# Optimization experiments

Hardware: AMD Instinct MI355X
Metric: run time of the kernel (lower is better)

## Reference

```python
import jax, jax.numpy as jnp
import numpy as np

NUM_RAYS = 4096
NUM_SAMPLES = 64
NUM_IMPORTANCE = 64
UPSAMPLE_STEPS = 4
HIDDEN = 128
SAMPLE_DIST = 2.0 / NUM_SAMPLES
COS_ANNEAL_RATIO = 0.0


def sdf_fn(params, pts):
    # pts: [P,3] -> sdf: [P,1]  (stand-in for sdf_network.get_sdf_vals)
    W1, b1, W2, b2, W3, b3 = params
    h = jax.nn.softplus(pts @ W1 + b1)
    h = jax.nn.softplus(h @ W2 + b2)
    return h @ W3 + b3


def sdf_grad(params, pts):
    # gradient of sdf w.r.t. points, [P,3] (stand-in for sdf_network.gradient)
    return jax.grad(lambda p: sdf_fn(params, p).sum())(pts)


def sample_pdf(bins, weights, n_samples):
    # deterministic inverse-transform sampling (det=True branch)
    weights = weights + 1e-5
    pdf = weights / jnp.sum(weights, axis=-1, keepdims=True)
    cdf = jnp.cumsum(pdf, axis=-1)
    cdf = jnp.concatenate([jnp.zeros_like(cdf[..., :1]), cdf], axis=-1)  # [N,S]
    u = jnp.linspace(0.5 / n_samples, 1.0 - 0.5 / n_samples, n_samples, dtype=cdf.dtype)
    u = jnp.broadcast_to(u, cdf.shape[:-1] + (n_samples,))
    inds = jax.vmap(lambda c, uu: jnp.searchsorted(c, uu, side='right'))(cdf, u)
    below = jnp.maximum(inds - 1, 0)
    above = jnp.minimum(inds, cdf.shape[-1] - 1)
    cdf_b = jnp.take_along_axis(cdf, below, axis=-1)
    cdf_a = jnp.take_along_axis(cdf, above, axis=-1)
    bins_b = jnp.take_along_axis(bins, below, axis=-1)
    bins_a = jnp.take_along_axis(bins, above, axis=-1)
    denom = cdf_a - cdf_b
    denom = jnp.where(denom < 1e-5, jnp.ones_like(denom), denom)
    t = (u - cdf_b) / denom
    return bins_b + t * (bins_a - bins_b)


def upsample(rays_o, rays_d, z_vals, sdf, n_importance, inv_s):
    N, S = z_vals.shape
    pts = rays_o[:, None, :] + rays_d[:, None, :] * z_vals[..., None]  # [N,S,3]
    radius = jnp.linalg.norm(pts, axis=-1)
    inside_sphere = ((radius[:, :-1] < 1.0) | (radius[:, 1:] < 1.0)).astype(z_vals.dtype)
    prev_sdf, next_sdf = sdf[:, :-1], sdf[:, 1:]
    prev_z, next_z = z_vals[:, :-1], z_vals[:, 1:]
    mid_sdf = (prev_sdf + next_sdf) * 0.5
    cos_val = (next_sdf - prev_sdf) / (next_z - prev_z + 1e-5)
    prev_cos = jnp.concatenate([jnp.zeros((N, 1), z_vals.dtype), cos_val[:, :-1]], axis=-1)
    cos_val = jnp.minimum(prev_cos, cos_val)
    cos_val = jnp.clip(cos_val, -1000.0, 0.0) * inside_sphere
    dist = next_z - prev_z
    prev_cdf = jax.nn.sigmoid((mid_sdf - cos_val * dist * 0.5) * inv_s)
    next_cdf = jax.nn.sigmoid((mid_sdf + cos_val * dist * 0.5) * inv_s)
    alpha = (prev_cdf - next_cdf + 1e-5) / (prev_cdf + 1e-5)
    trans = jnp.cumprod(jnp.concatenate([jnp.ones((N, 1), z_vals.dtype), 1.0 - alpha + 1e-7], axis=-1), axis=-1)[:, :-1]
    weights = alpha * trans
    return sample_pdf(z_vals, weights, n_importance)


def cat_z_vals(params, rays_o, rays_d, z_vals, new_z_vals, sdf, last):
    N = z_vals.shape[0]
    z_cat = jnp.concatenate([z_vals, new_z_vals], axis=-1)
    order = jnp.argsort(z_cat, axis=-1)
    z_sorted = jnp.take_along_axis(z_cat, order, axis=-1)
    if not last:
        pts = rays_o[:, None, :] + rays_d[:, None, :] * new_z_vals[..., None]
        new_sdf = sdf_fn(params, pts.reshape(-1, 3)).reshape(N, new_z_vals.shape[-1])
        sdf = jnp.take_along_axis(jnp.concatenate([sdf, new_sdf], axis=-1), order, axis=-1)
    return z_sorted, sdf


def render_depth(params, variance, rays_o, rays_d, sample_dist, z_vals):
    N, S = z_vals.shape
    dists = z_vals[..., 1:] - z_vals[..., :-1]
    dists = jnp.concatenate([dists, jnp.full((N, 1), sample_dist, z_vals.dtype)], axis=-1)
    mid_z = z_vals + dists * 0.5
    pts = (rays_o[:, None, :] + rays_d[:, None, :] * mid_z[..., None]).reshape(-1, 3)
    dirs = jnp.broadcast_to(rays_d[:, None, :], (N, S, 3)).reshape(-1, 3)
    sdf = sdf_fn(params, pts)              # [P,1]
    gradients = sdf_grad(params, pts)      # [P,3]
    inv_s = jnp.clip(jnp.exp(10.0 * variance), 1e-6, 1e6)
    true_cos = jnp.sum(dirs * gradients, axis=-1, keepdims=True)
    iter_cos = -(jax.nn.relu(-true_cos * 0.5 + 0.5) * (1.0 - COS_ANNEAL_RATIO)
                 + jax.nn.relu(-true_cos) * COS_ANNEAL_RATIO)
    d = dists.reshape(-1, 1)
    prev_cdf = jax.nn.sigmoid((sdf - iter_cos * d * 0.5) * inv_s)
    next_cdf = jax.nn.sigmoid((sdf + iter_cos * d * 0.5) * inv_s)
    alpha = jnp.clip((prev_cdf - next_cdf + 1e-5) / (prev_cdf + 1e-5), 0.0, 1.0).reshape(N, S)
    trans = jnp.cumprod(jnp.concatenate([jnp.ones((N, 1), z_vals.dtype), 1.0 - alpha + 1e-7], axis=-1), axis=-1)[:, :-1]
    weights = alpha * trans
    depths = jnp.sum(weights * z_vals, axis=-1)
    return depths, gradients


def setup_inputs():
    key = jax.random.key(0)
    ks = jax.random.split(key, 8)
    rays_o = 0.1 * jax.random.normal(ks[0], (NUM_RAYS, 3), jnp.float32)
    rd = jax.random.normal(ks[1], (NUM_RAYS, 3), jnp.float32)
    rays_d = rd / jnp.linalg.norm(rd, axis=-1, keepdims=True)
    near = 0.3 + 0.2 * jax.random.uniform(ks[2], (NUM_RAYS, 1), jnp.float32)
    far = near + 1.5
    W1 = jax.random.normal(ks[3], (3, HIDDEN), jnp.float32) / np.sqrt(3.0)
    W2 = jax.random.normal(ks[4], (HIDDEN, HIDDEN), jnp.float32) / np.sqrt(HIDDEN)
    W3 = jax.random.normal(ks[5], (HIDDEN, 1), jnp.float32) / np.sqrt(HIDDEN)
    b1 = jnp.zeros((HIDDEN,), jnp.float32)
    b2 = jnp.zeros((HIDDEN,), jnp.float32)
    b3 = jnp.zeros((1,), jnp.float32)
    variance = jnp.asarray(0.3, jnp.float32)
    return {"rays_o": rays_o, "rays_d": rays_d, "near": near, "far": far,
            "W1": W1, "b1": b1, "W2": W2, "b2": b2, "W3": W3, "b3": b3,
            "variance": variance}


def reference(rays_o, rays_d, near, far, W1, b1, W2, b2, W3, b3, variance):
    params = (W1, b1, W2, b2, W3, b3)
    N = rays_o.shape[0]
    z = jnp.linspace(0.0, 1.0, NUM_SAMPLES, dtype=jnp.float32)
    z_vals = near + (far - near) * z[None, :]  # [N,S0]
    # importance sampling (torch.no_grad block)
    pts = rays_o[:, None, :] + rays_d[:, None, :] * z_vals[..., None]
    sdf = sdf_fn(params, pts.reshape(-1, 3)).reshape(N, NUM_SAMPLES)
    n_imp = NUM_IMPORTANCE // UPSAMPLE_STEPS
    for i in range(UPSAMPLE_STEPS):
        new_z = upsample(rays_o, rays_d, z_vals, sdf, n_imp, 64.0 * (2 ** i))
        z_vals, sdf = cat_z_vals(params, rays_o, rays_d, z_vals, new_z, sdf,
                                 last=(i + 1 == UPSAMPLE_STEPS))
    z_vals = jax.lax.stop_gradient(z_vals)
    return render_depth(params, variance, rays_o, rays_d, SAMPLE_DIST, z_vals)
```

## Files before the change

kernel.cpp:

```cpp
#include <hip/hip_runtime.h>
#include <math.h>

#define HID 128
#define NRAYS 4096
#define TP 64

typedef __bf16 bf16x8 __attribute__((ext_vector_type(8)));
typedef float f32x4 __attribute__((ext_vector_type(4)));
typedef unsigned int uint32x4 __attribute__((ext_vector_type(4)));

union frag_u { bf16x8 v; uint32x4 q; };

__device__ __forceinline__ unsigned f2bf(float f){
  unsigned u = __float_as_uint(f);
  u += 0x7FFFu + ((u >> 16) & 1u);
  return u >> 16;
}
__device__ __forceinline__ float bf2f(unsigned h){
  return __uint_as_float(h << 16);
}
__device__ __forceinline__ float sp_fast(float x){
  float e = __expf(-fabsf(x));
  return fmaxf(x, 0.0f) + __logf(1.0f + e);
}
__device__ __forceinline__ float sg_fast(float x){
  float e = __expf(-fabsf(x));
  float r = __builtin_amdgcn_rcpf(1.0f + e);
  return (x >= 0.0f ? 1.0f : e) * r;
}
__device__ __forceinline__ float sg_f(float x){
  return 1.0f / (1.0f + expf(-x));
}
__device__ __forceinline__ f32x4 splat4(float x){
  f32x4 v = {x, x, x, x};
  return v;
}

#define SW(p,k) ((((p)*HID) + (k)) ^ (((p)&7)<<3))

__global__ void k_make_frags(const float* __restrict__ W2,
    unsigned short* __restrict__ w2fh,  unsigned short* __restrict__ w2fl,
    unsigned short* __restrict__ w2tfh, unsigned short* __restrict__ w2tfl){
  int idx = blockIdx.x*256 + threadIdx.x;
  if (idx >= 4096) return;
  int which = idx >> 11;
  int f    = (idx >> 6) & 31;
  int lane = idx & 63;
  int kc = f >> 3, tg = f & 7;
  int lg = lane >> 4, lr = lane & 15;
  unsigned short* dh = which ? w2tfh : w2fh;
  unsigned short* dl = which ? w2tfl : w2fl;
  int base = (f*64 + lane)*8;
  #pragma unroll
  for (int e = 0; e < 8; e++){
    int a = 32*kc + 8*lg + e;
    int b = 16*tg + lr;
    float v = which ? W2[b*HID + a] : W2[a*HID + b];
    unsigned hi = f2bf(v);
    dh[base+e] = (unsigned short)hi;
    dl[base+e] = (unsigned short)f2bf(v - bf2f(hi));
  }
}

__global__ void k_make_frags3(const float* __restrict__ W2,
    unsigned short* __restrict__ dh, unsigned short* __restrict__ dm,
    unsigned short* __restrict__ dl){
  int idx = blockIdx.x*256 + threadIdx.x;
  if (idx >= 2048) return;
  int f    = idx >> 6;
  int lane = idx & 63;
  int kc = f >> 3, tg = f & 7;
  int lg = lane >> 4, lr = lane & 15;
  int base = (f*64 + lane)*8;
  #pragma unroll
  for (int e = 0; e < 8; e++){
    int a = 32*kc + 8*lg + e;
    int b = 16*tg + lr;
    float v = W2[a*HID + b];
    unsigned hi = f2bf(v);
    float rm = v - bf2f(hi);
    unsigned md = f2bf(rm);
    dh[base+e] = (unsigned short)hi;
    dm[base+e] = (unsigned short)md;
    dl[base+e] = (unsigned short)f2bf(rm - bf2f(md));
  }
}

__global__ void k_init(const float* __restrict__ rays_o, const float* __restrict__ rays_d,
                       const float* __restrict__ nearv, const float* __restrict__ farv,
                       float* __restrict__ z_buf, float* __restrict__ pts){
  int idx = blockIdx.x*256 + threadIdx.x;
  if (idx >= NRAYS*64) return;
  int ray = idx >> 6, j = idx & 63;
  float nr = nearv[ray];
  float z = nr + (farv[ray] - nr) * ((float)j / 63.0f);
  z_buf[ray*128 + j] = z;
  pts[idx*3+0] = rays_o[ray*3+0] + rays_d[ray*3+0]*z;
  pts[idx*3+1] = rays_o[ray*3+1] + rays_d[ray*3+1]*z;
  pts[idx*3+2] = rays_o[ray*3+2] + rays_d[ray*3+2]*z;
}

__global__ __launch_bounds__(256, 3) void k_mlp_fwd_t(
    const float* __restrict__ pts,
    const float* __restrict__ W1, const float* __restrict__ b1,
    const float* __restrict__ b2,
    const float* __restrict__ W3, const float* __restrict__ b3,
    const unsigned short* __restrict__ w2h, const unsigned short* __restrict__ w2m,
    const unsigned short* __restrict__ w2l,
    float* __restrict__ sdf_out, const int* __restrict__ slots, int mode)
{
  __shared__ unsigned short sHi[64*HID];
  __shared__ unsigned short sMi[64*HID];
  __shared__ unsigned short sLo[64*HID];
  __shared__ float sRed[4][64];

  const int tid = threadIdx.x;
  const int l   = tid & 63;
  const int wv  = __builtin_amdgcn_readfirstlane(tid >> 6);
  const int lg  = l >> 4;
  const int lr  = l & 15;
  const int q0  = blockIdx.x * 64;
  const int kb  = 32*wv;

  const float x0 = pts[(q0+l)*3+0];
  const float x1 = pts[(q0+l)*3+1];
  const float x2 = pts[(q0+l)*3+2];

  #pragma unroll
  for (int g = 0; g < 4; g++){
    unsigned hw[4], mw[4], lw[4];
    #pragma unroll
    for (int e2 = 0; e2 < 4; e2++){
      unsigned hpk[2], mpk[2], lpk[2];
      #pragma unroll
      for (int t = 0; t < 2; t++){
        int k = kb + 8*g + 2*e2 + t;
        float pre = b1[k];
        pre = fmaf(x0, W1[k],       pre);
        pre = fmaf(x1, W1[HID+k],   pre);
        pre = fmaf(x2, W1[2*HID+k], pre);
        float h = sp_fast(pre);
        unsigned hi = f2bf(h);
        float rm = h - bf2f(hi);
        unsigned md = f2bf(rm);
        hpk[t] = hi; mpk[t] = md;
        lpk[t] = f2bf(rm - bf2f(md));
      }
      hw[e2] = hpk[0] | (hpk[1] << 16);
      mw[e2] = mpk[0] | (mpk[1] << 16);
      lw[e2] = lpk[0] | (lpk[1] << 16);
    }
    uint32x4 hq = {hw[0], hw[1], hw[2], hw[3]};
    uint32x4 mq = {mw[0], mw[1], mw[2], mw[3]};
    uint32x4 lq = {lw[0], lw[1], lw[2], lw[3]};
    *(uint32x4*)&sHi[SW(l, kb + 8*g)] = hq;
    *(uint32x4*)&sMi[SW(l, kb + 8*g)] = mq;
    *(uint32x4*)&sLo[SW(l, kb + 8*g)] = lq;
  }
  __syncthreads();

  f32x4 acc[4][2], accC[4][2];
  {
    const float b2a = b2[kb + lr];
    const float b2b = b2[kb + 16 + lr];
    #pragma unroll
    for (int mt = 0; mt < 4; mt++){
      acc[mt][0]  = splat4(b2a);
      acc[mt][1]  = splat4(b2b);
      accC[mt][0] = splat4(0.0f);
      accC[mt][1] = splat4(0.0f);
    }
  }
  #pragma unroll
  for (int kc = 0; kc < 4; kc++){
    frag_u bh0, bm0, bl0, bh1, bm1, bl1;
    const int f0 = ((kc*8 + 2*wv + 0)*64 + l)*8;
    const int f1 = ((kc*8 + 2*wv + 1)*64 + l)*8;
    bh0.q = *(const uint32x4*)(w2h + f0);
    bm0.q = *(const uint32x4*)(w2m + f0);
    bl0.q = *(const uint32x4*)(w2l + f0);
    bh1.q = *(const uint32x4*)(w2h + f1);
    bm1.q = *(const uint32x4*)(w2m + f1);
    bl1.q = *(const uint32x4*)(w2l + f1);
    const int kk = 32*kc + 8*lg;
    #pragma unroll
    for (int mt = 0; mt < 4; mt++){
      frag_u ah, am, al;
      ah.q = *(const uint32x4*)&sHi[SW(16*mt + lr, kk)];
      am.q = *(const uint32x4*)&sMi[SW(16*mt + lr, kk)];
      al.q = *(const uint32x4*)&sLo[SW(16*mt + lr, kk)];
      accC[mt][0] = __builtin_amdgcn_mfma_f32_16x16x32_bf16(ah.v, bl0.v, accC[mt][0], 0,0,0);
      accC[mt][0] = __builtin_amdgcn_mfma_f32_16x16x32_bf16(am.v, bm0.v, accC[mt][0], 0,0,0);
      accC[mt][0] = __builtin_amdgcn_mfma_f32_16x16x32_bf16(al.v, bh0.v, accC[mt][0], 0,0,0);
      accC[mt][0] = __builtin_amdgcn_mfma_f32_16x16x32_bf16(ah.v, bm0.v, accC[mt][0], 0,0,0);
      accC[mt][0] = __builtin_amdgcn_mfma_f32_16x16x32_bf16(am.v, bh0.v, accC[mt][0], 0,0,0);
      acc[mt][0]  = __builtin_amdgcn_mfma_f32_16x16x32_bf16(ah.v, bh0.v, acc[mt][0],  0,0,0);
      accC[mt][1] = __builtin_amdgcn_mfma_f32_16x16x32_bf16(ah.v, bl1.v, accC[mt][1], 0,0,0);
      accC[mt][1] = __builtin_amdgcn_mfma_f32_16x16x32_bf16(am.v, bm1.v, accC[mt][1], 0,0,0);
      accC[mt][1] = __builtin_amdgcn_mfma_f32_16x16x32_bf16(al.v, bh1.v, accC[mt][1], 0,0,0);
      accC[mt][1] = __builtin_amdgcn_mfma_f32_16x16x32_bf16(ah.v, bm1.v, accC[mt][1], 0,0,0);
      accC[mt][1] = __builtin_amdgcn_mfma_f32_16x16x32_bf16(am.v, bh1.v, accC[mt][1], 0,0,0);
      acc[mt][1]  = __builtin_amdgcn_mfma_f32_16x16x32_bf16(ah.v, bh1.v, acc[mt][1],  0,0,0);
    }
  }

  {
    const float w3a = W3[kb + lr];
    const float w3b = W3[kb + 16 + lr];
    #pragma unroll
    for (int mt = 0; mt < 4; mt++){
      float svr[4];
      #pragma unroll
      for (int r = 0; r < 4; r++){
        float pa = acc[mt][0][r] + accC[mt][0][r];
        float pb = acc[mt][1][r] + accC[mt][1][r];
        svr[r] = sp_fast(pa)*w3a + sp_fast(pb)*w3b;
      }
      #pragma unroll
      for (int m = 1; m < 16; m <<= 1){
        svr[0] += __shfl_xor(svr[0], m);
        svr[1] += __shfl_xor(svr[1], m);
        svr[2] += __shfl_xor(svr[2], m);
        svr[3] += __shfl_xor(svr[3], m);
      }
      if (lr == 0){
        sRed[wv][16*mt + 4*lg + 0] = svr[0];
        sRed[wv][16*mt + 4*lg + 1] = svr[1];
        sRed[wv][16*mt + 4*lg + 2] = svr[2];
        sRed[wv][16*mt + 4*lg + 3] = svr[3];
      }
    }
  }
  __syncthreads();
  if (tid < 64){
    float sv = b3[0] + sRed[0][tid] + sRed[1][tid] + sRed[2][tid] + sRed[3][tid];
    if (mode == 0){
      sdf_out[q0 + tid] = sv;
    } else if (mode == 1){
      sdf_out[(q0 << 1) + tid] = sv;
    } else {
      int p = q0 + tid;
      sdf_out[(p >> 4)*128 + slots[p]] = sv;
    }
  }
}

__global__ __launch_bounds__(256, 4) void k_mlp_bwd(
    const float* __restrict__ z_buf,
    const float* __restrict__ rays_o, const float* __restrict__ rays_d,
    const float* __restrict__ W1, const float* __restrict__ b1,
    const float* __restrict__ b2,
    const float* __restrict__ W3, const float* __restrict__ b3,
    const unsigned short* __restrict__ w2fh,  const unsigned short* __restrict__ w2fl,
    const unsigned short* __restrict__ w2tfh,
    float* __restrict__ sdf_out, float* __restrict__ grad_out)
{
  __shared__ unsigned short sHi[64*HID];
  __shared__ unsigned short sLo[64*HID];
  __shared__ float sRed[4][64];
  __shared__ float sPts[64][4];
  __shared__ float sGrad[4][64][3];

  const int tid = threadIdx.x;
  const int l   = tid & 63;
  const int wv  = __builtin_amdgcn_readfirstlane(tid >> 6);
  const int lg  = l >> 4;
  const int lr  = l & 15;
  const int q0  = blockIdx.x * 64;
  const int kb  = 32*wv;

  const int ray = q0 >> 7;
  const int s   = (q0 & 127) + l;
  const float z  = z_buf[q0 + l];
  const float zn = z_buf[q0 + l + ((s < 127) ? 1 : 0)];
  const float d  = (s < 127) ? (zn - z) : 0.03125f;
  const float midz = z + 0.5f*d;
  const float x0 = rays_o[ray*3+0] + rays_d[ray*3+0]*midz;
  const float x1 = rays_o[ray*3+1] + rays_d[ray*3+1]*midz;
  const float x2 = rays_o[ray*3+2] + rays_d[ray*3+2]*midz;
  if (wv == 0){ sPts[l][0] = x0; sPts[l][1] = x1; sPts[l][2] = x2; }

  #pragma unroll
  for (int g = 0; g < 4; g++){
    unsigned hw[4], lw[4];
    #pragma unroll
    for (int e2 = 0; e2 < 4; e2++){
      unsigned hpk[2], lpk[2];
      #pragma unroll
      for (int t = 0; t < 2; t++){
        int k = kb + 8*g + 2*e2 + t;
        float pre = b1[k];
        pre = fmaf(x0, W1[k],       pre);
        pre = fmaf(x1, W1[HID+k],   pre);
        pre = fmaf(x2, W1[2*HID+k], pre);
        float h = sp_fast(pre);
        unsigned hi = __float_as_uint(h) >> 16;
        float rm = h - __uint_as_float(hi << 16);
        hpk[t] = hi;
        lpk[t] = __float_as_uint(rm) >> 16;
      }
      hw[e2] = hpk[0] | (hpk[1] << 16);
      lw[e2] = lpk[0] | (lpk[1] << 16);
    }
    uint32x4 hq = {hw[0], hw[1], hw[2], hw[3]};
    uint32x4 lq = {lw[0], lw[1], lw[2], lw[3]};
    *(uint32x4*)&sHi[SW(l, kb + 8*g)] = hq;
    *(uint32x4*)&sLo[SW(l, kb + 8*g)] = lq;
  }
  __syncthreads();

  f32x4 acc[4][2];
  {
    const float b2a = b2[kb + lr];
    const float b2b = b2[kb + 16 + lr];
    #pragma unroll
    for (int mt = 0; mt < 4; mt++){
      acc[mt][0] = splat4(b2a);
      acc[mt][1] = splat4(b2b);
    }
  }
  #pragma unroll
  for (int kc = 0; kc < 4; kc++){
    frag_u bh0, bl0, bh1, bl1;
    const int f0 = ((kc*8 + 2*wv + 0)*64 + l)*8;
    const int f1 = ((kc*8 + 2*wv + 1)*64 + l)*8;
    bh0.q = *(const uint32x4*)(w2fh + f0);
    bl0.q = *(const uint32x4*)(w2fl + f0);
    bh1.q = *(const uint32x4*)(w2fh + f1);
    bl1.q = *(const uint32x4*)(w2fl + f1);
    const int kk = 32*kc + 8*lg;
    #pragma unroll
    for (int mt = 0; mt < 4; mt++){
      frag_u ah, al;
      ah.q = *(const uint32x4*)&sHi[SW(16*mt + lr, kk)];
      al.q = *(const uint32x4*)&sLo[SW(16*mt + lr, kk)];
      acc[mt][0] = __builtin_amdgcn_mfma_f32_16x16x32_bf16(ah.v, bh0.v, acc[mt][0], 0,0,0);
      acc[mt][0] = __builtin_amdgcn_mfma_f32_16x16x32_bf16(ah.v, bl0.v, acc[mt][0], 0,0,0);
      acc[mt][0] = __builtin_amdgcn_mfma_f32_16x16x32_bf16(al.v, bh0.v, acc[mt][0], 0,0,0);
      acc[mt][1] = __builtin_amdgcn_mfma_f32_16x16x32_bf16(ah.v, bh1.v, acc[mt][1], 0,0,0);
      acc[mt][1] = __builtin_amdgcn_mfma_f32_16x16x32_bf16(ah.v, bl1.v, acc[mt][1], 0,0,0);
      acc[mt][1] = __builtin_amdgcn_mfma_f32_16x16x32_bf16(al.v, bh1.v, acc[mt][1], 0,0,0);
    }
  }
  __syncthreads();

  {
    const float w3a = W3[kb + lr];
    const float w3b = W3[kb + 16 + lr];
    #pragma unroll
    for (int mt = 0; mt < 4; mt++){
      float svr[4];
      #pragma unroll
      for (int r = 0; r < 4; r++){
        float pa = acc[mt][0][r], pb = acc[mt][1][r];
        svr[r] = sp_fast(pa)*w3a + sp_fast(pb)*w3b;
        int pr = 16*mt + 4*lg + r;
        float ga = sg_fast(pa) * w3a;
        float gb = sg_fast(pb) * w3b;
        sHi[SW(pr, kb + lr)]      = (unsigned short)(__float_as_uint(ga) >> 16);
        sHi[SW(pr, kb + 16 + lr)] = (unsigned short)(__float_as_uint(gb) >> 16);
      }
      #pragma unroll
      for (int m = 1; m < 16; m <<= 1){
        svr[0] += __shfl_xor(svr[0], m);
        svr[1] += __shfl_xor(svr[1], m);
        svr[2] += __shfl_xor(svr[2], m);
        svr[3] += __shfl_xor(svr[3], m);
      }
      if (lr == 0){
        sRed[wv][16*mt + 4*lg + 0] = svr[0];
        sRed[wv][16*mt + 4*lg + 1] = svr[1];
        sRed[wv][16*mt + 4*lg + 2] = svr[2];
        sRed[wv][16*mt + 4*lg + 3] = svr[3];
      }
    }
  }
  __syncthreads();
  if (tid < 64)
    sdf_out[q0+tid] = b3[0] + sRed[0][tid] + sRed[1][tid] + sRed[2][tid] + sRed[3][tid];

  f32x4 acc2[4][2];
  #pragma unroll
  for (int pt = 0; pt < 4; pt++){
    acc2[pt][0] = splat4(0.0f);
    acc2[pt][1] = splat4(0.0f);
  }
  #pragma unroll
  for (int kcn = 0; kcn < 4; kcn++){
    frag_u ah0, ah1;
    const int f0 = ((kcn*8 + 2*wv + 0)*64 + l)*8;
    const int f1 = ((kcn*8 + 2*wv + 1)*64 + l)*8;
    ah0.q = *(const uint32x4*)(w2tfh + f0);
    ah1.q = *(const uint32x4*)(w2tfh + f1);
    const int nn = 32*kcn + 8*lg;
    #pragma unroll
    for (int pt = 0; pt < 4; pt++){
      frag_u bh;
      bh.q = *(const uint32x4*)&sHi[SW(16*pt + lr, nn)];
      acc2[pt][0] = __builtin_amdgcn_mfma_f32_16x16x32_bf16(ah0.v, bh.v, acc2[pt][0], 0,0,0);
      acc2[pt][1] = __builtin_amdgcn_mfma_f32_16x16x32_bf16(ah1.v, bh.v, acc2[pt][1], 0,0,0);
    }
  }

  {
    float w1a[2][4], w1b[2][4], w1c[2][4], b1v[2][4];
    #pragma unroll
    for (int t = 0; t < 2; t++)
      #pragma unroll
      for (int r = 0; r < 4; r++){
        int k = kb + 16*t + 4*lg + r;
        w1a[t][r] = W1[k]; w1b[t][r] = W1[HID+k]; w1c[t][r] = W1[2*HID+k];
        b1v[t][r] = b1[k];
      }
    #pragma unroll
    for (int pt = 0; pt < 4; pt++){
      const int p = 16*pt + lr;
      const float xx = sPts[p][0], xy = sPts[p][1], xz = sPts[p][2];
      float gx = 0.f, gy = 0.f, gz = 0.f;
      #pragma unroll
      for (int t = 0; t < 2; t++){
        #pragma unroll
        for (int r = 0; r < 4; r++){
          float pre1 = fmaf(xx, w1a[t][r], fmaf(xy, w1b[t][r], fmaf(xz, w1c[t][r], b1v[t][r])));
          float dp = acc2[pt][t][r] * sg_fast(pre1);
          gx = fmaf(w1a[t][r], dp, gx);
          gy = fmaf(w1b[t][r], dp, gy);
          gz = fmaf(w1c[t][r], dp, gz);
        }
      }
      gx += __shfl_xor(gx, 16); gx += __shfl_xor(gx, 32);
      gy += __shfl_xor(gy, 16); gy += __shfl_xor(gy, 32);
      gz += __shfl_xor(gz, 16); gz += __shfl_xor(gz, 32);
      if (lg == 0){
        sGrad[wv][p][0] = gx; sGrad[wv][p][1] = gy; sGrad[wv][p][2] = gz;
      }
    }
  }
  __syncthreads();
  if (tid < 64){
    #pragma unroll
    for (int c = 0; c < 3; c++)
      grad_out[(q0+tid)*3+c] =
        sGrad[0][tid][c] + sGrad[1][tid][c] + sGrad[2][tid][c] + sGrad[3][tid][c];
  }
}

__global__ __launch_bounds__(64) void k_upsample(
      const float* __restrict__ rays_o, const float* __restrict__ rays_d,
      float* __restrict__ z_buf, float* __restrict__ sdf_buf,
      float* __restrict__ pts_new, int* __restrict__ slots,
      int S, float inv_s, int last){
  __shared__ float z[128], sd[128], rad[128], cosv[128], alf[128], wv[128], cdf[129], nz[16];
  __shared__ int slt[16];
  const int ray = blockIdx.x;
  const int l   = threadIdx.x;
  const float ox = rays_o[ray*3], oy = rays_o[ray*3+1], oz = rays_o[ray*3+2];
  const float dx = rays_d[ray*3], dy = rays_d[ray*3+1], dz = rays_d[ray*3+2];
  for (int j = l; j < S; j += 64){
    float zz = z_buf[ray*128+j];
    z[j]  = zz;
    sd[j] = sdf_buf[ray*128+j];
    float px = ox+dx*zz, py = oy+dy*zz, pz = oz+dz*zz;
    rad[j] = sqrtf(px*px + py*py + pz*pz);
  }
  __syncthreads();
  for (int j = l; j < S-1; j += 64)
    cosv[j] = (sd[j+1]-sd[j]) / (z[j+1]-z[j] + 1e-5f);
  __syncthreads();
  for (int j = l; j < S-1; j += 64){
    float cv = fminf((j > 0) ? cosv[j-1] : 0.0f, cosv[j]);
    cv = fminf(fmaxf(cv, -1000.0f), 0.0f);
    float inside = (rad[j] < 1.0f || rad[j+1] < 1.0f) ? 1.0f : 0.0f;
    cv *= inside;
    float mid  = 0.5f*(sd[j]+sd[j+1]);
    float dist = z[j+1]-z[j];
    float e = sg_f((mid - cv*dist*0.5f)*inv_s);
    float f = sg_f((mid + cv*dist*0.5f)*inv_s);
    alf[j] = (e - f + 1e-5f) / (e + 1e-5f);
  }
  __syncthreads();
  if (l == 0){
    float T = 1.0f, wsum = 0.0f;
    for (int j = 0; j < S-1; j++){
      float w = alf[j]*T + 1e-5f;
      wv[j] = w; wsum += w;
      T *= (1.0f - alf[j] + 1e-7f);
    }
    cdf[0] = 0.0f;
    float c = 0.0f;
    for (int j = 0; j < S-1; j++){ c += wv[j]/wsum; cdf[j+1] = c; }
  }
  __syncthreads();
  if (l < 16){
    float u = 0.03125f + 0.0625f*(float)l;
    int idx = 0;
    while (idx < S && cdf[idx] <= u) idx++;
    int below = idx - 1; if (below < 0) below = 0;
    int above = (idx < S-1) ? idx : (S-1);
    float cb = cdf[below], ca = cdf[above];
    float den = ca - cb; if (den < 1e-5f) den = 1.0f;
    float t = (u - cb) / den;
    nz[l] = z[below] + t*(z[above] - z[below]);
  }
  __syncthreads();
  if (l == 0){
    int i = S-1, j = 15;
    for (int dst = S+15; dst >= 0; --dst){
      bool takeOld = (j < 0) || (i >= 0 && z[i] > nz[j]);
      if (takeOld){ z[dst] = z[i]; sd[dst] = sd[i]; i--; }
      else        { z[dst] = nz[j]; slt[j] = dst; j--; }
    }
  }
  __syncthreads();
  for (int j = l; j < S+16; j += 64){
    z_buf[ray*128+j]  = z[j];
    sdf_buf[ray*128+j] = sd[j];
  }
  if (!last && l < 16){
    slots[ray*16+l] = slt[l];
    float zz = nz[l];
    pts_new[(ray*16+l)*3+0] = ox + dx*zz;
    pts_new[(ray*16+l)*3+1] = oy + dy*zz;
    pts_new[(ray*16+l)*3+2] = oz + dz*zz;
  }
}

__global__ __launch_bounds__(64) void k_render(
    const float* __restrict__ z_buf, const float* __restrict__ sdf_mid,
    const float* __restrict__ rays_d, const float* __restrict__ grad,
    const float* __restrict__ variance, float* __restrict__ depth_out){
  const int ray = blockIdx.x;
  const int l   = threadIdx.x;
  float inv_s = expf(10.0f * variance[0]);
  inv_s = fminf(fmaxf(inv_s, 1e-6f), 1e6f);
  const float dx = rays_d[ray*3], dy = rays_d[ray*3+1], dz = rays_d[ray*3+2];
  const int i0 = ray*128 + 2*l, i1 = i0 + 1;
  const float z0 = z_buf[i0], z1 = z_buf[i1];
  const float zn1 = __shfl_down(z0, 1);
  const float d0 = z1 - z0;
  const float d1 = (l < 63) ? (zn1 - z1) : 0.03125f;
  float a0, a1;
  {
    float sdf = sdf_mid[i0];
    float gx = grad[i0*3], gy = grad[i0*3+1], gz = grad[i0*3+2];
    float tc = dx*gx + dy*gy + dz*gz;
    float ic = -fmaxf(0.5f - 0.5f*tc, 0.0f);
    float e = sg_fast((sdf - ic*d0*0.5f)*inv_s);
    float f = sg_fast((sdf + ic*d0*0.5f)*inv_s);
    a0 = fminf(fmaxf((e - f + 1e-5f) / (e + 1e-5f), 0.0f), 1.0f);
  }
  {
    float sdf = sdf_mid[i1];
    float gx = grad[i1*3], gy = grad[i1*3+1], gz = grad[i1*3+2];
    float tc = dx*gx + dy*gy + dz*gz;
    float ic = -fmaxf(0.5f - 0.5f*tc, 0.0f);
    float e = sg_fast((sdf - ic*d1*0.5f)*inv_s);
    float f = sg_fast((sdf + ic*d1*0.5f)*inv_s);
    a1 = fminf(fmaxf((e - f + 1e-5f) / (e + 1e-5f), 0.0f), 1.0f);
  }
  const float f0 = 1.0f - a0 + 1e-7f;
  const float f1 = 1.0f - a1 + 1e-7f;
  float incl = f0 * f1;
  #pragma unroll
  for (int off = 1; off < 64; off <<= 1){
    float t = __shfl_up(incl, off);
    if (l >= off) incl *= t;
  }
  float P = __shfl_up(incl, 1);
  if (l == 0) P = 1.0f;
  float part = P * (a0*z0 + f0*a1*z1);
  #pragma unroll
  for (int m = 1; m < 64; m <<= 1) part += __shfl_xor(part, m);
  if (l == 0) depth_out[ray] = part;
}

extern "C" void kernel_launch(void* const* d_in, const int* in_sizes, int n_in,
                              void* d_out, int out_size, void* d_ws, size_t ws_size,
                              hipStream_t stream){
  (void)in_sizes; (void)n_in; (void)out_size; (void)ws_size;
  const float* rays_o = (const float*)d_in[0];
  const float* rays_d = (const float*)d_in[1];
  const float* nearv  = (const float*)d_in[2];
  const float* farv   = (const float*)d_in[3];
  const float* W1 = (const float*)d_in[4];
  const float* b1 = (const float*)d_in[5];
  const float* W2 = (const float*)d_in[6];
  const float* b2 = (const float*)d_in[7];
  const float* W3 = (const float*)d_in[8];
  const float* b3 = (const float*)d_in[9];
  const float* variance = (const float*)d_in[10];

  float* ws      = (float*)d_ws;
  float* z_buf   = ws;
  float* sdf_buf = ws + 524288;
  float* sdf_tmp = ws + 1048576;
  int*   slots   = (int*)(ws + 1589248);
  unsigned short* w2fh  = (unsigned short*)(ws + 524288);
  unsigned short* w2fl  = w2fh + 16384;
  unsigned short* w2tfh = w2fh + 32768;
  unsigned short* w2tfl = w2fh + 49152;
  unsigned short* w2h3 = (unsigned short*)(ws + 1310720);
  unsigned short* w2m3 = w2h3 + 16384;
  unsigned short* w2l3 = w2h3 + 32768;

  float* out       = (float*)d_out;
  float* depth_out = out;
  float* grad_out  = out + NRAYS;
  float* pts       = grad_out;

  k_make_frags3<<<dim3(8), dim3(256), 0, stream>>>(W2, w2h3, w2m3, w2l3);
  k_init<<<dim3(1024), dim3(256), 0, stream>>>(rays_o, rays_d, nearv, farv, z_buf, pts);
  k_mlp_fwd_t<<<dim3(4096), dim3(256), 0, stream>>>(pts, W1,b1,b2,W3,b3,
                                                    w2h3,w2m3,w2l3, sdf_buf, nullptr, 1);

  for (int i = 0; i < 4; i++){
    int S = 64 + 16*i;
    float inv_s = (float)(64 << i);
    int last = (i == 3) ? 1 : 0;
    k_upsample<<<dim3(4096), dim3(64), 0, stream>>>(rays_o, rays_d, z_buf, sdf_buf,
                                                    pts, slots, S, inv_s, last);
    if (!last){
      k_mlp_fwd_t<<<dim3(1024), dim3(256), 0, stream>>>(pts, W1,b1,b2,W3,b3,
                                                        w2h3,w2m3,w2l3, sdf_buf, slots, 2);
    }
  }

  k_make_frags<<<dim3(16), dim3(256), 0, stream>>>(W2, w2fh, w2fl, w2tfh, w2tfl);
  k_mlp_bwd<<<dim3(8192), dim3(256), 0, stream>>>(z_buf, rays_o, rays_d,
                                                  W1,b1,b2,W3,b3,
                                                  w2fh,w2fl,w2tfh, sdf_tmp, grad_out);
  k_render<<<dim3(4096), dim3(64), 0, stream>>>(z_buf, sdf_tmp, rays_d, grad_out,
                                                variance, depth_out);
}
```

Measured before the change: 544.7 us.

## Fuse ray init into first MLP pass and use hardware bf16 conversions

Removes the separate k_init kernel. The first forward MLP pass (mode 1) now computes the initial z values and sample points directly from near/far and the ray data, and writes z_buf itself. Manual round-to-nearest bf16 packing and truncation are replaced with native __bf16 casts, which may map to hardware conversion instructions. The softplus and sigmoid evaluations in the backward kernel now share one exp per value. The truncations that became rounded conversions slightly change numerics in the split-precision backward path.

Result: no change. 540.8 us (-0.7%).

```diff
diff --git a/kernel.cpp b/kernel.cpp
--- a/kernel.cpp
+++ b/kernel.cpp
@@ -18,6 +18,11 @@
 }
 __device__ __forceinline__ float bf2f(unsigned h){
   return __uint_as_float(h << 16);
+}
+__device__ __forceinline__ unsigned short bfc(float f){
+  union { __bf16 b; unsigned short u; } c;
+  c.b = (__bf16)f;
+  return c.u;
 }
 __device__ __forceinline__ float sp_fast(float x){
   float e = __expf(-fabsf(x));
@@ -86,22 +91,11 @@
   }
 }
 
-__global__ void k_init(const float* __restrict__ rays_o, const float* __restrict__ rays_d,
-                       const float* __restrict__ nearv, const float* __restrict__ farv,
-                       float* __restrict__ z_buf, float* __restrict__ pts){
-  int idx = blockIdx.x*256 + threadIdx.x;
-  if (idx >= NRAYS*64) return;
-  int ray = idx >> 6, j = idx & 63;
-  float nr = nearv[ray];
-  float z = nr + (farv[ray] - nr) * ((float)j / 63.0f);
-  z_buf[ray*128 + j] = z;
-  pts[idx*3+0] = rays_o[ray*3+0] + rays_d[ray*3+0]*z;
-  pts[idx*3+1] = rays_o[ray*3+1] + rays_d[ray*3+1]*z;
-  pts[idx*3+2] = rays_o[ray*3+2] + rays_d[ray*3+2]*z;
-}
-
 __global__ __launch_bounds__(256, 3) void k_mlp_fwd_t(
     const float* __restrict__ pts,
+    const float* __restrict__ rays_o, const float* __restrict__ rays_d,
+    const float* __restrict__ nearv, const float* __restrict__ farv,
+    float* __restrict__ z_buf,
     const float* __restrict__ W1, const float* __restrict__ b1,
     const float* __restrict__ b2,
     const float* __restrict__ W3, const float* __restrict__ b3,
@@ -122,16 +116,27 @@
   const int q0  = blockIdx.x * 64;
   const int kb  = 32*wv;
 
-  const float x0 = pts[(q0+l)*3+0];
-  const float x1 = pts[(q0+l)*3+1];
-  const float x2 = pts[(q0+l)*3+2];
+  float x0, x1, x2;
+  if (mode == 1){
+    const int ray = blockIdx.x;
+    float nr = nearv[ray];
+    float z  = nr + (farv[ray] - nr) * ((float)l / 63.0f);
+    x0 = rays_o[ray*3+0] + rays_d[ray*3+0]*z;
+    x1 = rays_o[ray*3+1] + rays_d[ray*3+1]*z;
+    x2 = rays_o[ray*3+2] + rays_d[ray*3+2]*z;
+    if (wv == 0) z_buf[ray*128 + l] = z;
+  } else {
+    x0 = pts[(q0+l)*3+0];
+    x1 = pts[(q0+l)*3+1];
+    x2 = pts[(q0+l)*3+2];
+  }
 
   #pragma unroll
   for (int g = 0; g < 4; g++){
     unsigned hw[4], mw[4], lw[4];
     #pragma unroll
     for (int e2 = 0; e2 < 4; e2++){
-      unsigned hpk[2], mpk[2], lpk[2];
+      unsigned short hpk[2], mpk[2], lpk[2];
       #pragma unroll
       for (int t = 0; t < 2; t++){
         int k = kb + 8*g + 2*e2 + t;
@@ -140,15 +145,15 @@
         pre = fmaf(x1, W1[HID+k],   pre);
         pre = fmaf(x2, W1[2*HID+k], pre);
         float h = sp_fast(pre);
-        unsigned hi = f2bf(h);
-        float rm = h - bf2f(hi);
-        unsigned md = f2bf(rm);
-        hpk[t] = hi; mpk[t] = md;
-        lpk[t] = f2bf(rm - bf2f(md));
-      }
-      hw[e2] = hpk[0] | (hpk[1] << 16);
-      mw[e2] = mpk[0] | (mpk[1] << 16);
-      lw[e2] = lpk[0] | (lpk[1] << 16);
+        unsigned short hh = bfc(h);
+        float rm = h - bf2f(hh);
+        unsigned short mm = bfc(rm);
+        hpk[t] = hh; mpk[t] = mm;
+        lpk[t] = bfc(rm - bf2f(mm));
+      }
+      hw[e2] = (unsigned)hpk[0] | ((unsigned)hpk[1] << 16);
+      mw[e2] = (unsigned)mpk[0] | ((unsigned)mpk[1] << 16);
+      lw[e2] = (unsigned)lpk[0] | ((unsigned)lpk[1] << 16);
     }
     uint32x4 hq = {hw[0], hw[1], hw[2], hw[3]};
     uint32x4 mq = {mw[0], mw[1], mw[2], mw[3]};
@@ -285,7 +290,7 @@
     unsigned hw[4], lw[4];
     #pragma unroll
     for (int e2 = 0; e2 < 4; e2++){
-      unsigned hpk[2], lpk[2];
+      unsigned short hpk[2], lpk[2];
       #pragma unroll
       for (int t = 0; t < 2; t++){
         int k = kb + 8*g + 2*e2 + t;
@@ -294,13 +299,12 @@
         pre = fmaf(x1, W1[HID+k],   pre);
         pre = fmaf(x2, W1[2*HID+k], pre);
         float h = sp_fast(pre);
-        unsigned hi = __float_as_uint(h) >> 16;
-        float rm = h - __uint_as_float(hi << 16);
-        hpk[t] = hi;
-        lpk[t] = __float_as_uint(rm) >> 16;
-      }
-      hw[e2] = hpk[0] | (hpk[1] << 16);
-      lw[e2] = lpk[0] | (lpk[1] << 16);
+        unsigned short hh = bfc(h);
+        hpk[t] = hh;
+        lpk[t] = bfc(h - bf2f(hh));
+      }
+      hw[e2] = (unsigned)hpk[0] | ((unsigned)hpk[1] << 16);
+      lw[e2] = (unsigned)lpk[0] | ((unsigned)lpk[1] << 16);
     }
     uint32x4 hq = {hw[0], hw[1], hw[2], hw[3]};
     uint32x4 lq = {lw[0], lw[1], lw[2], lw[3]};
@@ -353,12 +357,16 @@
       #pragma unroll
       for (int r = 0; r < 4; r++){
         float pa = acc[mt][0][r], pb = acc[mt][1][r];
-        svr[r] = sp_fast(pa)*w3a + sp_fast(pb)*w3b;
+        float ea = __expf(-fabsf(pa)), eb = __expf(-fabsf(pb));
+        float ta = 1.0f + ea,          tb = 1.0f + eb;
+        float spa = fmaxf(pa, 0.0f) + __logf(ta);
+        float spb = fmaxf(pb, 0.0f) + __logf(tb);
+        svr[r] = spa*w3a + spb*w3b;
+        float sga = (pa >= 0.0f ? 1.0f : ea) * __builtin_amdgcn_rcpf(ta);
+        float sgb = (pb >= 0.0f ? 1.0f : eb) * __builtin_amdgcn_rcpf(tb);
         int pr = 16*mt + 4*lg + r;
-        float ga = sg_fast(pa) * w3a;
-        float gb = sg_fast(pb) * w3b;
-        sHi[SW(pr, kb + lr)]      = (unsigned short)(__float_as_uint(ga) >> 16);
-        sHi[SW(pr, kb + 16 + lr)] = (unsigned short)(__float_as_uint(gb) >> 16);
+        sHi[SW(pr, kb + lr)]      = bfc(sga * w3a);
+        sHi[SW(pr, kb + 16 + lr)] = bfc(sgb * w3b);
       }
       #pragma unroll
       for (int m = 1; m < 16; m <<= 1){
@@ -609,8 +617,8 @@
   float* pts       = grad_out;
 
   k_make_frags3<<<dim3(8), dim3(256), 0, stream>>>(W2, w2h3, w2m3, w2l3);
-  k_init<<<dim3(1024), dim3(256), 0, stream>>>(rays_o, rays_d, nearv, farv, z_buf, pts);
-  k_mlp_fwd_t<<<dim3(4096), dim3(256), 0, stream>>>(pts, W1,b1,b2,W3,b3,
+  k_mlp_fwd_t<<<dim3(4096), dim3(256), 0, stream>>>(pts, rays_o, rays_d, nearv, farv,
+                                                    z_buf, W1,b1,b2,W3,b3,
                                                     w2h3,w2m3,w2l3, sdf_buf, nullptr, 1);
 
   for (int i = 0; i < 4; i++){
@@ -620,7 +628,8 @@
     k_upsample<<<dim3(4096), dim3(64), 0, stream>>>(rays_o, rays_d, z_buf, sdf_buf,
                                                     pts, slots, S, inv_s, last);
     if (!last){
-      k_mlp_fwd_t<<<dim3(1024), dim3(256), 0, stream>>>(pts, W1,b1,b2,W3,b3,
+      k_mlp_fwd_t<<<dim3(1024), dim3(256), 0, stream>>>(pts, rays_o, rays_d, nearv, farv,
+                                                        z_buf, W1,b1,b2,W3,b3,
                                                         w2h3,w2m3,w2l3, sdf_buf, slots, 2);
     }
   }
```
